# Performance work log

Measured on AMD Instinct MI355X. Metric: run time of the kernel, lower is better.

Reference implementation:

```python
import jax, jax.numpy as jnp
import numpy as np

N, D, H, E = 50000, 128, 128, 800000


def setup_inputs() -> dict:
    key = jax.random.key(0)
    ks = jax.random.split(key, 12)
    p = lambda k, shape: jax.random.normal(k, shape, dtype=jnp.float32) * 0.02
    z = lambda n: jnp.zeros((n,), jnp.float32)
    return {
        "x1": jax.random.normal(ks[0], (N, D), dtype=jnp.float32),
        "edge_index1": jax.random.randint(ks[1], (2, E), 0, N, dtype=jnp.int32),
        "x2": jax.random.normal(ks[2], (N, D), dtype=jnp.float32),
        "edge_index2": jax.random.randint(ks[3], (2, E), 0, N, dtype=jnp.int32),
        "enc_w1": p(ks[4], (D, H)), "enc_b1": z(H),
        "enc_w2": p(ks[5], (H, H)), "enc_b2": z(H),
        "conv1_w": p(ks[6], (H, H)), "conv1_b": z(H),
        "conv2_w": p(ks[7], (H, H)), "conv2_b": z(H),
        "sim_w1": p(ks[8], (4 * H, H)), "sim_b1": z(H),
        "sim_w2": p(ks[9], (H, 1)), "sim_b2": z(1),
    }


def reference(x1, edge_index1, x2, edge_index2,
              enc_w1, enc_b1, enc_w2, enc_b2,
              conv1_w, conv1_b, conv2_w, conv2_b,
              sim_w1, sim_b1, sim_w2, sim_b2):
    def gcn(x, ei, W, b):
        row, col = ei[0], ei[1]            # [E], [E]
        h = x @ W + b                      # [N, H]
        n = x.shape[0]
        deg = jax.ops.segment_sum(jnp.ones(row.shape[0], h.dtype), row, num_segments=n)
        dis = jnp.where(deg > 0, deg ** -0.5, 0.0)   # deg^-0.5, inf -> 0
        norm = dis[row] * dis[col]         # [E]
        msg = h[col] * norm[:, None]       # gather + per-edge scale, [E, H]
        return jax.ops.segment_sum(msg, row, num_segments=n)  # scatter-add

    def embed(x, ei):
        h = jax.nn.relu(x @ enc_w1 + enc_b1) @ enc_w2 + enc_b2  # encoder MLP
        h = jax.nn.relu(gcn(h, ei, conv1_w, conv1_b))
        h = jax.nn.relu(gcn(h, ei, conv2_w, conv2_b))
        return h.mean(axis=0)              # mean pooling -> [H]

    g1 = embed(x1, edge_index1)
    g2 = embed(x2, edge_index2)
    c = jnp.concatenate([g1, g2, jnp.abs(g1 - g2), g1 * g2], axis=-1)  # [4H]
    return jax.nn.relu(c @ sim_w1 + sim_b1) @ sim_w2 + sim_b2          # [1]
```

## Files before the change

kernel.cpp:

```cpp
#include <hip/hip_runtime.h>
#include <hip/hip_bf16.h>

#define HD 128

typedef _Float16 f16x8 __attribute__((ext_vector_type(8)));
typedef _Float16 f16x2 __attribute__((ext_vector_type(2)));
typedef float f32x4 __attribute__((ext_vector_type(4)));

__global__ void k_deg_slot(const int* __restrict__ ei0, const int* __restrict__ ei1,
                           int E, int N, int* __restrict__ deg2,
                           unsigned short* __restrict__ slot) {
  int g = blockIdx.y;
  const int* rows = (g ? ei1 : ei0);
  int base = (blockIdx.x * 256 + threadIdx.x) * 8;
  int* deg = deg2 + g * N;
  unsigned short* sl = slot + (size_t)g * E;
  if (base + 7 < E) {
    int4 r0 = *(const int4*)(rows + base);
    int4 r1 = *(const int4*)(rows + base + 4);
    union { unsigned short us[8]; uint4 v; } s;
    s.us[0] = (unsigned short)atomicAdd(&deg[r0.x], 1);
    s.us[1] = (unsigned short)atomicAdd(&deg[r0.y], 1);
    s.us[2] = (unsigned short)atomicAdd(&deg[r0.z], 1);
    s.us[3] = (unsigned short)atomicAdd(&deg[r0.w], 1);
    s.us[4] = (unsigned short)atomicAdd(&deg[r1.x], 1);
    s.us[5] = (unsigned short)atomicAdd(&deg[r1.y], 1);
    s.us[6] = (unsigned short)atomicAdd(&deg[r1.z], 1);
    s.us[7] = (unsigned short)atomicAdd(&deg[r1.w], 1);
    *(uint4*)(sl + base) = s.v;
  } else {
    for (int e = base; e < E; ++e)
      sl[e] = (unsigned short)atomicAdd(&deg[rows[e]], 1);
  }
}

__global__ void k_scan_block(const int* __restrict__ deg, int* __restrict__ offs,
                             int* __restrict__ partials, int Ntot) {
  __shared__ int s[256];
  int t = threadIdx.x;
  int i = blockIdx.x * 256 + t;
  int v = (i < Ntot) ? deg[i] : 0;
  s[t] = v;
  __syncthreads();
  #pragma unroll
  for (int off = 1; off < 256; off <<= 1) {
    int x = (t >= off) ? s[t - off] : 0;
    __syncthreads();
    s[t] += x;
    __syncthreads();
  }
  if (i < Ntot) offs[i] = s[t] - v;
  if (t == 255) partials[blockIdx.x] = s[255];
}

__global__ void k_scan_partials(int* __restrict__ partials, int P) {
  __shared__ int s[512];
  int t = threadIdx.x;
  int v = (t < P) ? partials[t] : 0;
  s[t] = v;
  __syncthreads();
  #pragma unroll
  for (int off = 1; off < 512; off <<= 1) {
    int x = (t >= off) ? s[t - off] : 0;
    __syncthreads();
    s[t] += x;
    __syncthreads();
  }
  if (t < P) partials[t] = s[t] - v;
}

__global__ void k_scan_finalize(int* __restrict__ offs, const int* __restrict__ partials,
                                const int* __restrict__ deg, float* __restrict__ dis,
                                int Ntot, int Etot) {
  int i = blockIdx.x * 256 + threadIdx.x;
  if (i < Ntot) {
    offs[i] += partials[blockIdx.x];
    int d = deg[i];
    dis[i] = (d > 0) ? (1.0f / sqrtf((float)d)) : 0.0f;
  }
  if (blockIdx.x == 0 && threadIdx.x == 0) offs[Ntot] = Etot;
}

__global__ void k_csr_fill(const int* __restrict__ ei0, const int* __restrict__ ei1,
                           int E, int N, const int* __restrict__ offs,
                           const unsigned short* __restrict__ slot,
                           unsigned short* __restrict__ csr_col) {
  int g = blockIdx.y;
  const int* eg = (g ? ei1 : ei0);
  const int* ob = offs + g * N;
  const unsigned short* sl = slot + (size_t)g * E;
  int base = (blockIdx.x * 256 + threadIdx.x) * 4;
  if (base + 3 < E) {
    int4 r = *(const int4*)(eg + base);
    int4 c = *(const int4*)(eg + E + base);
    uint2 sv = *(const uint2*)(sl + base);
    csr_col[ob[r.x] + (sv.x & 0xffff)] = (unsigned short)c.x;
    csr_col[ob[r.y] + (sv.x >> 16)]   = (unsigned short)c.y;
    csr_col[ob[r.z] + (sv.y & 0xffff)] = (unsigned short)c.z;
    csr_col[ob[r.w] + (sv.y >> 16)]   = (unsigned short)c.w;
  } else {
    for (int e = base; e < E; ++e)
      csr_col[ob[eg[e]] + sl[e]] = (unsigned short)eg[E + e];
  }
}

__global__ void k_cvt_w(const float* __restrict__ w0, const float* __restrict__ w1,
                        const float* __restrict__ w2, const float* __restrict__ w3,
                        _Float16* __restrict__ Wf) {
  int m = blockIdx.x >> 6;
  const float* W = (m == 0) ? w0 : (m == 1) ? w1 : (m == 2) ? w2 : w3;
  int idx = (blockIdx.x & 63) * 256 + threadIdx.x;
  int n = idx & 127, k = idx >> 7;
  float w = W[(size_t)k * HD + n];
  int nt = n >> 4, n16 = n & 15, kc = k >> 5, q = (k >> 3) & 3, j = k & 7;
  int lanei = 16 * q + n16;
  size_t off = ((size_t)(nt * 4 + kc) * 64 + lanei) * 8 + j;
  Wf[(size_t)m * 16384 + off] = (_Float16)w;
}

template<bool RELU, bool SCALE, bool CVT>
__global__ __launch_bounds__(256, 2) void k_gemm_lds(
    const _Float16* __restrict__ Ab,
    const float* __restrict__ Af0, const float* __restrict__ Af1,
    const _Float16* __restrict__ Wf, const float* __restrict__ bias,
    const float* __restrict__ scale, _Float16* __restrict__ C,
    int N, int Ntot) {
  __shared__ _Float16 lds[16384];
  const int tid = threadIdx.x;
  #pragma unroll
  for (int i = 0; i < 8; ++i)
    *(float4*)&lds[(size_t)(i * 256 + tid) * 8] = *(const float4*)&Wf[(size_t)(i * 256 + tid) * 8];
  __syncthreads();

  const int lane = tid & 63;
  const int wave = tid >> 6;
  const int n16 = lane & 15, q = lane >> 4;
  const int rowbase = blockIdx.x * 256 + wave * 64;

  int arow[4];
  #pragma unroll
  for (int t = 0; t < 4; ++t) {
    int r = rowbase + 16 * t + n16;
    arow[t] = (r < Ntot) ? r : (Ntot - 1);
  }

  f32x4 acc[4][8];
  #pragma unroll
  for (int t = 0; t < 4; ++t)
    #pragma unroll
    for (int nt = 0; nt < 8; ++nt) acc[t][nt] = (f32x4){0.f, 0.f, 0.f, 0.f};

  #pragma unroll
  for (int kc = 0; kc < 4; ++kc) {
    f16x8 a[4];
    #pragma unroll
    for (int t = 0; t < 4; ++t) {
      if (CVT) {
        int r = arow[t];
        const float* src = (r < N) ? (Af0 + (size_t)r * HD) : (Af1 + (size_t)(r - N) * HD);
        float4 u0 = *(const float4*)(src + kc * 32 + q * 8);
        float4 u1 = *(const float4*)(src + kc * 32 + q * 8 + 4);
        union { _Float16 h[8]; f16x8 v; } tmp;
        tmp.h[0] = (_Float16)u0.x; tmp.h[1] = (_Float16)u0.y;
        tmp.h[2] = (_Float16)u0.z; tmp.h[3] = (_Float16)u0.w;
        tmp.h[4] = (_Float16)u1.x; tmp.h[5] = (_Float16)u1.y;
        tmp.h[6] = (_Float16)u1.z; tmp.h[7] = (_Float16)u1.w;
        a[t] = tmp.v;
      } else {
        a[t] = *(const f16x8*)(Ab + (size_t)arow[t] * HD + kc * 32 + q * 8);
      }
    }
    #pragma unroll
    for (int nt = 0; nt < 8; ++nt) {
      f16x8 b = *(const f16x8*)&lds[(size_t)((nt * 4 + kc) * 64 + lane) * 8];
      #pragma unroll
      for (int t = 0; t < 4; ++t)
        acc[t][nt] = __builtin_amdgcn_mfma_f32_16x16x32_f16(a[t], b, acc[t][nt], 0, 0, 0);
    }
  }

  float bv[8];
  #pragma unroll
  for (int nt = 0; nt < 8; ++nt) bv[nt] = bias[nt * 16 + n16];

  #pragma unroll
  for (int t = 0; t < 4; ++t) {
    #pragma unroll
    for (int r = 0; r < 4; ++r) {
      int row = rowbase + 16 * t + 4 * q + r;
      if (row < Ntot) {
        float s = SCALE ? scale[row] : 1.0f;
        #pragma unroll
        for (int nt = 0; nt < 8; ++nt) {
          float v = acc[t][nt][r] + bv[nt];
          if (RELU) v = fmaxf(v, 0.f);
          if (SCALE) v *= s;
          C[(size_t)row * HD + nt * 16 + n16] = (_Float16)v;
        }
      }
    }
  }
}

template<bool POOL>
__global__ __launch_bounds__(256) void k_aggregate(
    const _Float16* __restrict__ T, const int* __restrict__ offs,
    const unsigned short* __restrict__ csr_col, const float* __restrict__ dis,
    _Float16* __restrict__ out, float* __restrict__ poolrep, int N, int Ntot) {
  __shared__ float red[4][128];
  const int lane = threadIdx.x & 63;
  const int wave = threadIdx.x >> 6;
  const int gw = blockIdx.x * 4 + wave;
  const int sub = lane >> 4, c16 = lane & 15;

  f16x2 hacc[4];
  #pragma unroll
  for (int j = 0; j < 4; ++j) hacc[j] = (f16x2){(_Float16)0.f, (_Float16)0.f};

  if (gw < Ntot) {
    const int beg = offs[gw], end = offs[gw + 1];
    const uint4* Tg = (const uint4*)(T + (size_t)(gw >= N ? N : 0) * HD);
    for (int e = beg; e < end; e += 16) {
      uint4 v[4];
      #pragma unroll
      for (int gp = 0; gp < 4; ++gp) {
        v[gp] = make_uint4(0, 0, 0, 0);
        if (e + 4 * gp < end) {
          int eg = e + 4 * gp + sub;
          bool valid = (eg < end);
          int ce = valid ? eg : (end - 1);
          int col = csr_col[ce];
          uint4 t = Tg[(size_t)col * 16 + c16];
          if (valid) v[gp] = t;
        }
      }
      #pragma unroll
      for (int gp = 0; gp < 4; ++gp) {
        union { uint4 u; f16x2 h[4]; } w;
        w.u = v[gp];
        hacc[0] += w.h[0];
        hacc[1] += w.h[1];
        hacc[2] += w.h[2];
        hacc[3] += w.h[3];
      }
    }
  }

  float ax[8];
  #pragma unroll
  for (int j = 0; j < 4; ++j) {
    ax[2 * j]     = (float)hacc[j][0];
    ax[2 * j + 1] = (float)hacc[j][1];
  }
  #pragma unroll
  for (int j = 0; j < 8; ++j) {
    ax[j] += __shfl_xor(ax[j], 32, 64);
    ax[j] += __shfl_xor(ax[j], 16, 64);
  }
  float dr = (gw < Ntot) ? dis[gw] : 0.f;
  #pragma unroll
  for (int j = 0; j < 8; ++j) ax[j] = fmaxf(ax[j] * dr, 0.f);

  if (!POOL) {
    if (gw < Ntot && sub == 0) {
      union { uint4 u; _Float16 h[8]; } o;
      #pragma unroll
      for (int j = 0; j < 8; ++j) o.h[j] = (_Float16)ax[j];
      ((uint4*)out)[(size_t)gw * 16 + c16] = o.u;
    }
  } else {
    if (sub == 0) {
      *(float4*)&red[wave][c16 * 8]     = make_float4(ax[0], ax[1], ax[2], ax[3]);
      *(float4*)&red[wave][c16 * 8 + 4] = make_float4(ax[4], ax[5], ax[6], ax[7]);
    }
    __syncthreads();
    int t = threadIdx.x;
    if (t < 128) {
      float s = red[0][t] + red[1][t] + red[2][t] + red[3][t];
      int g = (blockIdx.x * 4 >= N) ? 1 : 0;
      atomicAdd(&poolrep[(size_t)((blockIdx.x & 15) * 2 + g) * 128 + t], s);
    }
  }
}

__global__ void k_final(const float* __restrict__ poolrep,
                        const float* __restrict__ W1, const float* __restrict__ b1,
                        const float* __restrict__ W2, const float* __restrict__ b2,
                        float* __restrict__ out, float invN) {
  __shared__ float cs[512];
  __shared__ float red[2];
  int t = threadIdx.x;
  float g1 = 0.f, g2 = 0.f;
  #pragma unroll
  for (int r = 0; r < 16; ++r) {
    g1 += poolrep[r * 256 + t];
    g2 += poolrep[r * 256 + 128 + t];
  }
  g1 *= invN;
  g2 *= invN;
  cs[t] = g1;
  cs[128 + t] = g2;
  cs[256 + t] = fabsf(g1 - g2);
  cs[384 + t] = g1 * g2;
  __syncthreads();
  float acc = b1[t];
  #pragma unroll 8
  for (int i = 0; i < 512; ++i) acc = fmaf(cs[i], W1[(size_t)i * HD + t], acc);
  float h = fmaxf(acc, 0.f);
  float v = h * W2[t];
  #pragma unroll
  for (int off = 32; off > 0; off >>= 1) v += __shfl_down(v, off, 64);
  if ((t & 63) == 0) red[t >> 6] = v;
  __syncthreads();
  if (t == 0) out[0] = red[0] + red[1] + b2[0];
}

extern "C" void kernel_launch(void* const* d_in, const int* in_sizes, int n_in,
                              void* d_out, int out_size, void* d_ws, size_t ws_size,
                              hipStream_t stream) {
  const float* x1     = (const float*)d_in[0];
  const int*   ei1    = (const int*)d_in[1];
  const float* x2     = (const float*)d_in[2];
  const int*   ei2    = (const int*)d_in[3];
  const float* W_in[4] = {(const float*)d_in[4], (const float*)d_in[6],
                          (const float*)d_in[8], (const float*)d_in[10]};
  const float* B_in[4] = {(const float*)d_in[5], (const float*)d_in[7],
                          (const float*)d_in[9], (const float*)d_in[11]};
  const float* sim_w1 = (const float*)d_in[12];
  const float* sim_b1 = (const float*)d_in[13];
  const float* sim_w2 = (const float*)d_in[14];
  const float* sim_b2 = (const float*)d_in[15];

  const int N = in_sizes[0] / HD;
  const int E = in_sizes[1] / 2;
  const int Ntot = 2 * N;

  _Float16* sp = (_Float16*)d_ws;
  _Float16* bufA = sp; sp += (size_t)Ntot * HD;
  _Float16* bufB = sp; sp += (size_t)Ntot * HD;
  _Float16* Wf   = sp; sp += 4 * 16384;
  float* fp = (float*)sp;
  float* dis     = fp; fp += Ntot;
  float* poolrep = fp; fp += 16 * 256;
  int* ip = (int*)fp;
  int* deg2     = ip; ip += Ntot;
  int* offs     = ip; ip += Ntot + 1;
  int* partials = ip; ip += 512;
  ip = (int*)(((uintptr_t)ip + 15) & ~(uintptr_t)15);
  unsigned short* slot = (unsigned short*)ip;
  unsigned short* csr_col = slot + 2 * (size_t)E;

  const int scanBlocks = (Ntot + 255) / 256;
  const int gemmBlocks = (Ntot + 255) / 256;
  const int aggBlocks  = (Ntot + 3) / 4;
  const dim3 degGrid((E / 8 + 255) / 256, 2);
  const dim3 fillGrid((E / 4 + 255) / 256, 2);

  hipMemsetAsync(poolrep, 0, (16 * 256 + Ntot) * sizeof(float), stream);

  k_cvt_w<<<256, 256, 0, stream>>>(W_in[0], W_in[1], W_in[2], W_in[3], Wf);

  k_deg_slot<<<degGrid, 256, 0, stream>>>(ei1, ei2, E, N, deg2, slot);
  k_scan_block<<<scanBlocks, 256, 0, stream>>>(deg2, offs, partials, Ntot);
  k_scan_partials<<<1, 512, 0, stream>>>(partials, scanBlocks);
  k_scan_finalize<<<scanBlocks, 256, 0, stream>>>(offs, partials, deg2, dis, Ntot, 2 * E);
  k_csr_fill<<<fillGrid, 256, 0, stream>>>(ei1, ei2, E, N, offs, slot, csr_col);

  k_gemm_lds<true,  false, true ><<<gemmBlocks, 256, 0, stream>>>(
      nullptr, x1, x2, Wf + 0 * 16384, B_in[0], nullptr, bufA, N, Ntot);
  k_gemm_lds<false, false, false><<<gemmBlocks, 256, 0, stream>>>(
      bufA, nullptr, nullptr, Wf + 1 * 16384, B_in[1], nullptr, bufB, N, Ntot);
  k_gemm_lds<false, true,  false><<<gemmBlocks, 256, 0, stream>>>(
      bufB, nullptr, nullptr, Wf + 2 * 16384, B_in[2], dis, bufA, N, Ntot);
  k_aggregate<false><<<aggBlocks, 256, 0, stream>>>(bufA, offs, csr_col, dis, bufB, nullptr, N, Ntot);
  k_gemm_lds<false, true,  false><<<gemmBlocks, 256, 0, stream>>>(
      bufB, nullptr, nullptr, Wf + 3 * 16384, B_in[3], dis, bufA, N, Ntot);
  k_aggregate<true ><<<aggBlocks, 256, 0, stream>>>(bufA, offs, csr_col, dis, nullptr, poolrep, N, Ntot);

  k_final<<<1, 128, 0, stream>>>(poolrep, sim_w1, sim_b1, sim_w2, sim_b2,
                                 (float*)d_out, 1.0f / (float)N);
}
```

Baseline: 423.5 us.

## Fold CSR scan stages into GEMM launches and convert weights in-kernel

Removes the separate weight-conversion kernel: each GEMM block now loads fp32 weights and writes them as swizzled fp16 into LDS itself. The three scan kernels (block scan, partials scan, finalize) become extra blocks tacked onto the three encoder/conv GEMM launches, so they overlap with GEMM work, and the dis computation moves into the block-scan stage. The degree kernel now handles 4 edges per thread instead of 8, and the CSR fill runs after the third GEMM. This cuts the number of launches and serial small kernels, at the cost of every GEMM block redoing the fp32-to-fp16 weight conversion.

```diff
diff --git a/kernel.cpp b/kernel.cpp
--- a/kernel.cpp
+++ b/kernel.cpp
@@ -1,5 +1,4 @@
 #include <hip/hip_runtime.h>
-#include <hip/hip_bf16.h>
 
 #define HD 128
 
@@ -11,74 +10,22 @@
                            int E, int N, int* __restrict__ deg2,
                            unsigned short* __restrict__ slot) {
   int g = blockIdx.y;
-  const int* rows = (g ? ei1 : ei0);
-  int base = (blockIdx.x * 256 + threadIdx.x) * 8;
+  const int* rows = g ? ei1 : ei0;
   int* deg = deg2 + g * N;
   unsigned short* sl = slot + (size_t)g * E;
-  if (base + 7 < E) {
-    int4 r0 = *(const int4*)(rows + base);
-    int4 r1 = *(const int4*)(rows + base + 4);
-    union { unsigned short us[8]; uint4 v; } s;
-    s.us[0] = (unsigned short)atomicAdd(&deg[r0.x], 1);
-    s.us[1] = (unsigned short)atomicAdd(&deg[r0.y], 1);
-    s.us[2] = (unsigned short)atomicAdd(&deg[r0.z], 1);
-    s.us[3] = (unsigned short)atomicAdd(&deg[r0.w], 1);
-    s.us[4] = (unsigned short)atomicAdd(&deg[r1.x], 1);
-    s.us[5] = (unsigned short)atomicAdd(&deg[r1.y], 1);
-    s.us[6] = (unsigned short)atomicAdd(&deg[r1.z], 1);
-    s.us[7] = (unsigned short)atomicAdd(&deg[r1.w], 1);
-    *(uint4*)(sl + base) = s.v;
+  int base = (blockIdx.x * 256 + threadIdx.x) * 4;
+  if (base + 3 < E) {
+    int4 r = *(const int4*)(rows + base);
+    union { unsigned short us[4]; uint2 v; } s;
+    s.us[0] = (unsigned short)atomicAdd(&deg[r.x], 1);
+    s.us[1] = (unsigned short)atomicAdd(&deg[r.y], 1);
+    s.us[2] = (unsigned short)atomicAdd(&deg[r.z], 1);
+    s.us[3] = (unsigned short)atomicAdd(&deg[r.w], 1);
+    *(uint2*)(sl + base) = s.v;
   } else {
     for (int e = base; e < E; ++e)
       sl[e] = (unsigned short)atomicAdd(&deg[rows[e]], 1);
   }
-}
-
-__global__ void k_scan_block(const int* __restrict__ deg, int* __restrict__ offs,
-                             int* __restrict__ partials, int Ntot) {
-  __shared__ int s[256];
-  int t = threadIdx.x;
-  int i = blockIdx.x * 256 + t;
-  int v = (i < Ntot) ? deg[i] : 0;
-  s[t] = v;
-  __syncthreads();
-  #pragma unroll
-  for (int off = 1; off < 256; off <<= 1) {
-    int x = (t >= off) ? s[t - off] : 0;
-    __syncthreads();
-    s[t] += x;
-    __syncthreads();
-  }
-  if (i < Ntot) offs[i] = s[t] - v;
-  if (t == 255) partials[blockIdx.x] = s[255];
-}
-
-__global__ void k_scan_partials(int* __restrict__ partials, int P) {
-  __shared__ int s[512];
-  int t = threadIdx.x;
-  int v = (t < P) ? partials[t] : 0;
-  s[t] = v;
-  __syncthreads();
-  #pragma unroll
-  for (int off = 1; off < 512; off <<= 1) {
-    int x = (t >= off) ? s[t - off] : 0;
-    __syncthreads();
-    s[t] += x;
-    __syncthreads();
-  }
-  if (t < P) partials[t] = s[t] - v;
-}
-
-__global__ void k_scan_finalize(int* __restrict__ offs, const int* __restrict__ partials,
-                                const int* __restrict__ deg, float* __restrict__ dis,
-                                int Ntot, int Etot) {
-  int i = blockIdx.x * 256 + threadIdx.x;
-  if (i < Ntot) {
-    offs[i] += partials[blockIdx.x];
-    int d = deg[i];
-    dis[i] = (d > 0) ? (1.0f / sqrtf((float)d)) : 0.0f;
-  }
-  if (blockIdx.x == 0 && threadIdx.x == 0) offs[Ntot] = Etot;
 }
 
 __global__ void k_csr_fill(const int* __restrict__ ei0, const int* __restrict__ ei1,
@@ -95,47 +42,42 @@
     int4 c = *(const int4*)(eg + E + base);
     uint2 sv = *(const uint2*)(sl + base);
     csr_col[ob[r.x] + (sv.x & 0xffff)] = (unsigned short)c.x;
-    csr_col[ob[r.y] + (sv.x >> 16)]   = (unsigned short)c.y;
+    csr_col[ob[r.y] + (sv.x >> 16)]    = (unsigned short)c.y;
     csr_col[ob[r.z] + (sv.y & 0xffff)] = (unsigned short)c.z;
-    csr_col[ob[r.w] + (sv.y >> 16)]   = (unsigned short)c.w;
+    csr_col[ob[r.w] + (sv.y >> 16)]    = (unsigned short)c.w;
   } else {
     for (int e = base; e < E; ++e)
       csr_col[ob[eg[e]] + sl[e]] = (unsigned short)eg[E + e];
   }
 }
 
-__global__ void k_cvt_w(const float* __restrict__ w0, const float* __restrict__ w1,
-                        const float* __restrict__ w2, const float* __restrict__ w3,
-                        _Float16* __restrict__ Wf) {
-  int m = blockIdx.x >> 6;
-  const float* W = (m == 0) ? w0 : (m == 1) ? w1 : (m == 2) ? w2 : w3;
-  int idx = (blockIdx.x & 63) * 256 + threadIdx.x;
-  int n = idx & 127, k = idx >> 7;
-  float w = W[(size_t)k * HD + n];
-  int nt = n >> 4, n16 = n & 15, kc = k >> 5, q = (k >> 3) & 3, j = k & 7;
-  int lanei = 16 * q + n16;
-  size_t off = ((size_t)(nt * 4 + kc) * 64 + lanei) * 8 + j;
-  Wf[(size_t)m * 16384 + off] = (_Float16)w;
-}
-
 template<bool RELU, bool SCALE, bool CVT>
-__global__ __launch_bounds__(256, 2) void k_gemm_lds(
-    const _Float16* __restrict__ Ab,
-    const float* __restrict__ Af0, const float* __restrict__ Af1,
-    const _Float16* __restrict__ Wf, const float* __restrict__ bias,
-    const float* __restrict__ scale, _Float16* __restrict__ C,
-    int N, int Ntot) {
-  __shared__ _Float16 lds[16384];
+__device__ __forceinline__ void gemm_block(
+    _Float16* lds, int bi,
+    const _Float16* __restrict__ Ab, const float* __restrict__ Af0,
+    const float* __restrict__ Af1, const float* __restrict__ Wg,
+    const float* __restrict__ bias, const float* __restrict__ scale,
+    _Float16* __restrict__ C, int N, int Ntot) {
   const int tid = threadIdx.x;
   #pragma unroll
-  for (int i = 0; i < 8; ++i)
-    *(float4*)&lds[(size_t)(i * 256 + tid) * 8] = *(const float4*)&Wf[(size_t)(i * 256 + tid) * 8];
+  for (int i = 0; i < 16; ++i) {
+    int flat = i * 1024 + tid * 4;
+    int k = flat >> 7, n0 = flat & 127;
+    float4 w4 = *(const float4*)(Wg + flat);
+    int kc = k >> 5, q = (k >> 3) & 3, j = k & 7;
+    float wv[4] = {w4.x, w4.y, w4.z, w4.w};
+    #pragma unroll
+    for (int d = 0; d < 4; ++d) {
+      int n = n0 + d;
+      lds[(size_t)(((n >> 4) * 4 + kc) * 64 + 16 * q + (n & 15)) * 8 + j] = (_Float16)wv[d];
+    }
+  }
   __syncthreads();
 
   const int lane = tid & 63;
   const int wave = tid >> 6;
   const int n16 = lane & 15, q = lane >> 4;
-  const int rowbase = blockIdx.x * 256 + wave * 64;
+  const int rowbase = bi * 256 + wave * 64;
 
   int arow[4];
   #pragma unroll
@@ -199,6 +141,68 @@
         }
       }
     }
+  }
+}
+
+template<bool RELU, bool SCALE, bool CVT, int AUX>
+__global__ __launch_bounds__(256, 2) void k_gemm_aux(
+    const _Float16* __restrict__ Ab, const float* __restrict__ Af0,
+    const float* __restrict__ Af1, const float* __restrict__ Wg,
+    const float* __restrict__ bias, const float* __restrict__ scale,
+    _Float16* __restrict__ C, int N, int Ntot, int gemmBlocks,
+    const int* __restrict__ deg, int* __restrict__ offs,
+    int* __restrict__ partials, float* __restrict__ dis,
+    int scanBlocks, int Etot) {
+  __shared__ _Float16 lds[16384];
+  int bi = blockIdx.x;
+  if (bi < gemmBlocks) {
+    gemm_block<RELU, SCALE, CVT>(lds, bi, Ab, Af0, Af1, Wg, bias, scale, C, N, Ntot);
+    return;
+  }
+  int b = bi - gemmBlocks;
+  int t = threadIdx.x;
+  if (AUX == 1) {
+    int* s = (int*)lds;
+    int i = b * 256 + t;
+    int v = (i < Ntot) ? deg[i] : 0;
+    s[t] = v;
+    __syncthreads();
+    #pragma unroll
+    for (int off = 1; off < 256; off <<= 1) {
+      int x = (t >= off) ? s[t - off] : 0;
+      __syncthreads();
+      s[t] += x;
+      __syncthreads();
+    }
+    if (i < Ntot) {
+      offs[i] = s[t] - v;
+      dis[i] = (v > 0) ? (1.0f / sqrtf((float)v)) : 0.0f;
+    }
+    if (t == 255) partials[b] = s[255];
+  } else if (AUX == 2) {
+    int* s = (int*)lds;
+    int P = scanBlocks;
+    int v0 = (t < P) ? partials[t] : 0;
+    int v1 = (t + 256 < P) ? partials[t + 256] : 0;
+    s[t] = v0;
+    s[t + 256] = v1;
+    __syncthreads();
+    #pragma unroll
+    for (int off = 1; off < 256; off <<= 1) {
+      int x0 = (t >= off) ? s[t - off] : 0;
+      int x1 = (t >= off) ? s[256 + t - off] : 0;
+      __syncthreads();
+      s[t] += x0;
+      s[256 + t] += x1;
+      __syncthreads();
+    }
+    int tot0 = s[255];
+    if (t < P) partials[t] = s[t] - v0;
+    if (t + 256 < P) partials[t + 256] = s[256 + t] + tot0 - v1;
+  } else if (AUX == 3) {
+    int i = b * 256 + t;
+    if (i < Ntot) offs[i] += partials[b];
+    if (b == 0 && t == 0) offs[Ntot] = Etot;
   }
 }
 
@@ -338,7 +342,6 @@
   _Float16* sp = (_Float16*)d_ws;
   _Float16* bufA = sp; sp += (size_t)Ntot * HD;
   _Float16* bufB = sp; sp += (size_t)Ntot * HD;
-  _Float16* Wf   = sp; sp += 4 * 16384;
   float* fp = (float*)sp;
   float* dis     = fp; fp += Ntot;
   float* poolrep = fp; fp += 16 * 256;
@@ -350,32 +353,36 @@
   unsigned short* slot = (unsigned short*)ip;
   unsigned short* csr_col = slot + 2 * (size_t)E;
 
+  const int gemmBlocks = (Ntot + 255) / 256;
   const int scanBlocks = (Ntot + 255) / 256;
-  const int gemmBlocks = (Ntot + 255) / 256;
   const int aggBlocks  = (Ntot + 3) / 4;
-  const dim3 degGrid((E / 8 + 255) / 256, 2);
-  const dim3 fillGrid((E / 4 + 255) / 256, 2);
+  const dim3 edgeGrid(((E + 3) / 4 + 255) / 256, 2);
 
   hipMemsetAsync(poolrep, 0, (16 * 256 + Ntot) * sizeof(float), stream);
 
-  k_cvt_w<<<256, 256, 0, stream>>>(W_in[0], W_in[1], W_in[2], W_in[3], Wf);
-
-  k_deg_slot<<<degGrid, 256, 0, stream>>>(ei1, ei2, E, N, deg2, slot);
-  k_scan_block<<<scanBlocks, 256, 0, stream>>>(deg2, offs, partials, Ntot);
-  k_scan_partials<<<1, 512, 0, stream>>>(partials, scanBlocks);
-  k_scan_finalize<<<scanBlocks, 256, 0, stream>>>(offs, partials, deg2, dis, Ntot, 2 * E);
-  k_csr_fill<<<fillGrid, 256, 0, stream>>>(ei1, ei2, E, N, offs, slot, csr_col);
-
-  k_gemm_lds<true,  false, true ><<<gemmBlocks, 256, 0, stream>>>(
-      nullptr, x1, x2, Wf + 0 * 16384, B_in[0], nullptr, bufA, N, Ntot);
-  k_gemm_lds<false, false, false><<<gemmBlocks, 256, 0, stream>>>(
-      bufA, nullptr, nullptr, Wf + 1 * 16384, B_in[1], nullptr, bufB, N, Ntot);
-  k_gemm_lds<false, true,  false><<<gemmBlocks, 256, 0, stream>>>(
-      bufB, nullptr, nullptr, Wf + 2 * 16384, B_in[2], dis, bufA, N, Ntot);
+  k_deg_slot<<<edgeGrid, 256, 0, stream>>>(ei1, ei2, E, N, deg2, slot);
+
+  k_gemm_aux<true, false, true, 1><<<gemmBlocks + scanBlocks, 256, 0, stream>>>(
+      nullptr, x1, x2, W_in[0], B_in[0], nullptr, bufA, N, Ntot, gemmBlocks,
+      deg2, offs, partials, dis, scanBlocks, 2 * E);
+
+  k_gemm_aux<false, false, false, 2><<<gemmBlocks + 1, 256, 0, stream>>>(
+      bufA, nullptr, nullptr, W_in[1], B_in[1], nullptr, bufB, N, Ntot, gemmBlocks,
+      deg2, offs, partials, dis, scanBlocks, 2 * E);
+
+  k_gemm_aux<false, true, false, 3><<<gemmBlocks + scanBlocks, 256, 0, stream>>>(
+      bufB, nullptr, nullptr, W_in[2], B_in[2], dis, bufA, N, Ntot, gemmBlocks,
+      deg2, offs, partials, dis, scanBlocks, 2 * E);
+
+  k_csr_fill<<<edgeGrid, 256, 0, stream>>>(ei1, ei2, E, N, offs, slot, csr_col);
+
   k_aggregate<false><<<aggBlocks, 256, 0, stream>>>(bufA, offs, csr_col, dis, bufB, nullptr, N, Ntot);
-  k_gemm_lds<false, true,  false><<<gemmBlocks, 256, 0, stream>>>(
-      bufB, nullptr, nullptr, Wf + 3 * 16384, B_in[3], dis, bufA, N, Ntot);
-  k_aggregate<true ><<<aggBlocks, 256, 0, stream>>>(bufA, offs, csr_col, dis, nullptr, poolrep, N, Ntot);
+
+  k_gemm_aux<false, true, false, 0><<<gemmBlocks, 256, 0, stream>>>(
+      bufB, nullptr, nullptr, W_in[3], B_in[3], dis, bufA, N, Ntot, gemmBlocks,
+      deg2, offs, partials, dis, scanBlocks, 2 * E);
+
+  k_aggregate<true><<<aggBlocks, 256, 0, stream>>>(bufA, offs, csr_col, dis, nullptr, poolrep, N, Ntot);
 
   k_final<<<1, 128, 0, stream>>>(poolrep, sim_w1, sim_b1, sim_w2, sim_b2,
                                  (float*)d_out, 1.0f / (float)N);
```

After: 429.5 us. Within noise of the previous version (+1.4%).
